# Kernel tuning notes

Measured on AMD Instinct MI355X. Metric: run time of the kernel, lower is better.

The kernel has to match this reference:

```python
import jax, jax.numpy as jnp
import numpy as np

N = 65536      # nodes in batched graph
E = 2097152    # edges (avg degree 32)
V = 1000       # chord vocabulary size
F_IN = 128     # chord feature dim
H = 256        # hidden_dim
OUT = 128      # out_dim
G = 256        # number of graphs in batch


def _gcn_layer(x, W, b, row, col, norm, n):
    # x: [n, f_in] -> [n, f_out]; PyG GCNConv: linear then normalized aggregation + bias
    x = x @ W
    msg = x[row] * norm[:, None]            # gather at source, scale by sym-norm
    return jax.ops.segment_sum(msg, col, num_segments=n) + b


def setup_inputs() -> dict:
    key = jax.random.key(0)
    ks = jax.random.split(key, 9)
    chord_feats = jax.random.normal(ks[0], (V, F_IN), jnp.float32)
    W1 = jax.random.normal(ks[1], (F_IN, H), jnp.float32) * 0.05
    b1 = jnp.zeros((H,), jnp.float32)
    W2 = jax.random.normal(ks[2], (H, OUT), jnp.float32) * 0.05
    b2 = jnp.zeros((OUT,), jnp.float32)
    edge_attr = jax.random.uniform(ks[3], (E,), jnp.float32)          # positive edge weights
    node_indices = jax.random.randint(ks[4], (N,), 0, V, jnp.int64)
    edge_index = jax.random.randint(ks[5], (2, E), 0, N, jnp.int64)
    batch_index = jnp.sort(jax.random.randint(ks[6], (N,), 0, G, jnp.int64))
    return {"chord_feats": chord_feats, "W1": W1, "b1": b1, "W2": W2, "b2": b2,
            "edge_attr": edge_attr, "node_indices": node_indices,
            "edge_index": edge_index, "batch_index": batch_index}


def reference(chord_feats, W1, b1, W2, b2, edge_attr, node_indices, edge_index, batch_index):
    loops = jnp.arange(N, dtype=edge_index.dtype)
    row = jnp.concatenate([edge_index[0], loops])   # source
    col = jnp.concatenate([edge_index[1], loops])   # target
    ew = jnp.concatenate([edge_attr, jnp.ones((N,), edge_attr.dtype)])  # self-loop weight 1
    # symmetric GCN normalization: D^-1/2 A D^-1/2
    deg = jax.ops.segment_sum(ew, col, num_segments=N)
    dis = jnp.where(deg > 0, jax.lax.rsqrt(jnp.maximum(deg, 1e-30)), 0.0)
    norm = dis[row] * ew * dis[col]

    x = chord_feats[node_indices]                   # [N, F_IN]
    x = jax.nn.relu(_gcn_layer(x, W1, b1, row, col, norm, N))
    x = jax.nn.relu(_gcn_layer(x, W2, b2, row, col, norm, N))

    # global_mean_pool over batch_index
    sums = jax.ops.segment_sum(x, batch_index, num_segments=G)
    counts = jax.ops.segment_sum(jnp.ones((N,), x.dtype), batch_index, num_segments=G)
    return sums / jnp.maximum(counts, 1.0)[:, None]
```

## Files before the change

kernel.cpp:

```cpp
#include <hip/hip_runtime.h>
#include <hip/hip_fp16.h>
#include <math.h>

constexpr int N_NODES = 65536;
constexpr int N_EDGES = 2097152;
constexpr int F_IN    = 128;
constexpr int H_DIM   = 256;
constexpr int O_DIM   = 128;
constexpr int N_GRAPH = 256;
constexpr int V_SIZE  = 1000;

constexpr int EPB  = 8192;
constexpr int NBLK = N_EDGES / EPB;
constexpr float FXP = 16777216.0f;

typedef _Float16 half8 __attribute__((ext_vector_type(8)));
typedef float floatx4 __attribute__((ext_vector_type(4)));


__global__ void k_init(float* __restrict__ pool, const int* __restrict__ batch,
                       float* __restrict__ cntf, const float* __restrict__ cf,
                       const float* __restrict__ W1, __half* __restrict__ cfW1,
                       const float* __restrict__ W2, _Float16* __restrict__ W2T) {
    __shared__ float xs[8 * F_IN];
    int i = blockIdx.x * blockDim.x + threadIdx.x;
    if (i < N_GRAPH * O_DIM) pool[i] = 0.0f;
    if (blockIdx.x == 0) {
        int g = threadIdx.x;
        int lo = 0, hi = N_NODES;
        while (lo < hi) { int m = (lo + hi) >> 1; if (batch[m] < g) lo = m + 1; else hi = m; }
        int start = lo;
        lo = 0; hi = N_NODES;
        while (lo < hi) { int m = (lo + hi) >> 1; if (batch[m] <= g) lo = m + 1; else hi = m; }
        cntf[g] = (float)(lo - start);
    }
    if (blockIdx.x < V_SIZE / 8) {
        int rb = blockIdx.x * 8;
        int t  = threadIdx.x;
        #pragma unroll
        for (int p = 0; p < 4; ++p) {
            int idx = p * 256 + t;
            int r = idx >> 7, k = idx & 127;
            xs[idx] = cf[(size_t)(rb + r) * F_IN + k];
        }
        __syncthreads();
        float acc[8] = {};
        for (int k = 0; k < F_IN; ++k) {
            float w = W1[k * H_DIM + t];
            #pragma unroll
            for (int j = 0; j < 8; ++j) acc[j] += xs[j * F_IN + k] * w;
        }
        #pragma unroll
        for (int j = 0; j < 8; ++j)
            cfW1[(size_t)(rb + j) * H_DIM + t] = __float2half(acc[j]);
    }
    if (blockIdx.x >= 128) {
        int idx = (blockIdx.x - 128) * 256 + threadIdx.x;
        int nn = idx >> 8, kk = idx & 255;
        W2T[idx] = (_Float16)W2[kk * O_DIM + nn];
    }
}


__global__ void k_hist(const int* __restrict__ col, int* __restrict__ hist) {
    __shared__ int h[256];
    int t = threadIdx.x;
    if (t < 256) h[t] = 0;
    __syncthreads();
    int base = blockIdx.x * EPB;
    #pragma unroll
    for (int i = 0; i < EPB / 1024; ++i)
        atomicAdd(&h[col[base + i * 1024 + t] >> 8], 1);
    __syncthreads();
    if (t < 256) hist[t * NBLK + blockIdx.x] = h[t];
}


__global__ void k_scan1(const int* __restrict__ in, int* __restrict__ out,
                        int* __restrict__ bsum) {
    __shared__ int s[256];
    int tid = threadIdx.x;
    int i = blockIdx.x * 256 + tid;
    int v = in[i];
    s[tid] = v;
    __syncthreads();
    for (int d = 1; d < 256; d <<= 1) {
        int t = (tid >= d) ? s[tid - d] : 0;
        __syncthreads();
        s[tid] += t;
        __syncthreads();
    }
    out[i] = s[tid] - v;
    if (tid == 255) bsum[blockIdx.x] = s[255];
}

__global__ void k_scan2(int* __restrict__ bsum) {
    __shared__ int s[256];
    int tid = threadIdx.x;
    int v = bsum[tid];
    s[tid] = v;
    __syncthreads();
    for (int d = 1; d < 256; d <<= 1) {
        int t = (tid >= d) ? s[tid - d] : 0;
        __syncthreads();
        s[tid] += t;
        __syncthreads();
    }
    bsum[tid] = s[tid] - v;
}


__global__ void k_part(const int* __restrict__ row, const int* __restrict__ col,
                       const float* __restrict__ ew, const int* __restrict__ nidx,
                       const int* __restrict__ hoffs, const int* __restrict__ bsum,
                       int2* __restrict__ part) {
    __shared__ int cur[256];
    int t = threadIdx.x;
    if (t < 256) cur[t] = hoffs[t * NBLK + blockIdx.x] + bsum[t];
    __syncthreads();
    int base = blockIdx.x * EPB;
    #pragma unroll
    for (int i = 0; i < EPB / 1024; ++i) {
        int e = base + i * 1024 + t;
        int r = row[e], c = col[e];
        unsigned hw = (unsigned)__half_as_ushort(__float2half(ew[e]));
        int vb = nidx[r];
        int slot = atomicAdd(&cur[c >> 8], 1);
        int2 rec;
        rec.x = (r << 16) | ((c & 255) << 8) | (vb >> 2);
        rec.y = (int)(((unsigned)(vb & 3) << 16) | hw);
        part[slot] = rec;
    }
}


__global__ void k_build1(const int* __restrict__ hoffs, const int* __restrict__ bsum,
                         const int2* __restrict__ part, float* __restrict__ dis,
                         int* __restrict__ offs) {
    __shared__ unsigned long long dc[256];
    __shared__ int sc[256];
    int t = threadIdx.x;
    int bucket = blockIdx.x;
    if (t < 256) dc[t] = 0ULL;
    __syncthreads();
    int start = hoffs[bucket * NBLK] + bsum[bucket];
    int end   = (bucket == 255) ? N_EDGES : (hoffs[(bucket + 1) * NBLK] + bsum[bucket + 1]);
    for (int j = start + t; j < end; j += 1024) {
        int2 rec = part[j];
        int dst = (rec.x >> 8) & 255;
        float w = __half2float(__ushort_as_half((unsigned short)(rec.y & 0xFFFF)));
        atomicAdd(&dc[dst], (1ULL << 40) |
                  (unsigned long long)(unsigned)(w * FXP + 0.5f));
    }
    __syncthreads();
    unsigned long long v = (t < 256) ? dc[t] : 0ULL;
    if (t < 256) {
        float deg = 1.0f + (float)(v & 0xFFFFFFFFFFULL) * (1.0f / FXP);
        dis[bucket * 256 + t] = 1.0f / sqrtf(deg);
        sc[t] = (int)(v >> 40);
    }
    __syncthreads();
    for (int d = 1; d < 256; d <<= 1) {
        int x = (t >= d && t < 256) ? sc[t - d] : 0;
        __syncthreads();
        if (t < 256) sc[t] += x;
        __syncthreads();
    }
    if (t < 256) {
        int cnt = (int)(v >> 40);
        offs[bucket * 256 + t] = start + sc[t] - cnt;
    }
    if (bucket == 255 && t == 255) offs[N_NODES] = N_EDGES;
}


__global__ void k_build2(const int* __restrict__ hoffs, const int* __restrict__ bsum,
                         const int2* __restrict__ part, const float* __restrict__ dis,
                         const int* __restrict__ offs, int2* __restrict__ csr) {
    __shared__ int cur[256];
    int t = threadIdx.x;
    int bucket = blockIdx.x;
    if (t < 256) cur[t] = offs[bucket * 256 + t];
    __syncthreads();
    int start = hoffs[bucket * NBLK] + bsum[bucket];
    int end   = (bucket == 255) ? N_EDGES : (hoffs[(bucket + 1) * NBLK] + bsum[bucket + 1]);
    for (int j = start + t; j < end; j += 1024) {
        int2 rec = part[j];
        int dst = (rec.x >> 8) & 255;
        unsigned src = ((unsigned)rec.x) >> 16;
        int vb = ((rec.x & 255) << 2) | ((rec.y >> 16) & 3);
        float w = __half2float(__ushort_as_half((unsigned short)(rec.y & 0xFFFF)));
        float nm = dis[src] * w;
        int slot = atomicAdd(&cur[dst], 1);
        int2 e;
        e.x = (int)((src << 10) | (unsigned)vb);
        e.y = __float_as_int(nm);
        csr[slot] = e;
    }
}

__device__ __forceinline__ void acc8(float* e, int4 v, float n) {
    float2 f0 = __half22float2(*(__half2*)&v.x);
    float2 f1 = __half22float2(*(__half2*)&v.y);
    float2 f2 = __half22float2(*(__half2*)&v.z);
    float2 f3 = __half22float2(*(__half2*)&v.w);
    e[0] += f0.x * n; e[1] += f0.y * n;
    e[2] += f1.x * n; e[3] += f1.y * n;
    e[4] += f2.x * n; e[5] += f2.y * n;
    e[6] += f3.x * n; e[7] += f3.y * n;
}


__global__ void k_agg1(const int4* __restrict__ cfW1, const int* __restrict__ nidx,
                       const float* __restrict__ dis, const int* __restrict__ offs,
                       const int2* __restrict__ csr, const float4* __restrict__ b1f4,
                       int4* __restrict__ h1) {
    int wave = threadIdx.x >> 6;
    int lane = threadIdx.x & 63;
    int g    = lane >> 5;
    int sl   = lane & 31;
    int c = blockIdx.x * 4 + wave;
    float d = dis[c];
    int4 sp = cfW1[(size_t)nidx[c] * 32 + sl];
    float esum[8] = {0.f, 0.f, 0.f, 0.f, 0.f, 0.f, 0.f, 0.f};
    int a0 = offs[c], a1 = offs[c + 1];
    int s = a0;
    if (s < a1 && (s & 1)) {
        int sb = __builtin_amdgcn_readfirstlane(s);
        int2 e0 = csr[sb];
        int4 v0 = cfW1[(size_t)(e0.x & 1023) * 32 + sl];
        float n = (g == 0) ? __int_as_float(e0.y) : 0.0f;
        acc8(esum, v0, n);
        ++s;
    }
    for (; s + 8 <= a1; s += 8) {
        int sb = __builtin_amdgcn_readfirstlane(s);
        int4 ee[4];
        #pragma unroll
        for (int u = 0; u < 4; ++u) ee[u] = *(const int4*)(csr + sb + 2 * u);
        int4 v[4]; float n[4];
        #pragma unroll
        for (int u = 0; u < 4; ++u) {
            int ex = g ? ee[u].z : ee[u].x;
            int ey = g ? ee[u].w : ee[u].y;
            n[u] = __int_as_float(ey);
            v[u] = cfW1[(size_t)(ex & 1023) * 32 + sl];
        }
        #pragma unroll
        for (int u = 0; u < 4; ++u) acc8(esum, v[u], n[u]);
    }
    for (; s + 2 <= a1; s += 2) {
        int sb = __builtin_amdgcn_readfirstlane(s);
        int4 ee = *(const int4*)(csr + sb);
        int ex = g ? ee.z : ee.x;
        int ey = g ? ee.w : ee.y;
        int4 v0 = cfW1[(size_t)(ex & 1023) * 32 + sl];
        acc8(esum, v0, __int_as_float(ey));
    }
    if (s < a1) {
        int sb = __builtin_amdgcn_readfirstlane(s);
        int2 e0 = csr[sb];
        int4 v0 = cfW1[(size_t)(e0.x & 1023) * 32 + sl];
        float n = (g == 0) ? __int_as_float(e0.y) : 0.0f;
        acc8(esum, v0, n);
    }
    #pragma unroll
    for (int k = 0; k < 8; ++k) esum[k] += __shfl_xor(esum[k], 32, 64);

    float dd = d * d;
    float2 s0 = __half22float2(*(__half2*)&sp.x);
    float2 s1 = __half22float2(*(__half2*)&sp.y);
    float2 s2 = __half22float2(*(__half2*)&sp.z);
    float2 s3 = __half22float2(*(__half2*)&sp.w);
    float4 bb0 = b1f4[2 * sl];
    float4 bb1 = b1f4[2 * sl + 1];
    float r[8];
    r[0] = bb0.x + s0.x * dd + d * esum[0];
    r[1] = bb0.y + s0.y * dd + d * esum[1];
    r[2] = bb0.z + s1.x * dd + d * esum[2];
    r[3] = bb0.w + s1.y * dd + d * esum[3];
    r[4] = bb1.x + s2.x * dd + d * esum[4];
    r[5] = bb1.y + s2.y * dd + d * esum[5];
    r[6] = bb1.z + s3.x * dd + d * esum[6];
    r[7] = bb1.w + s3.y * dd + d * esum[7];
    #pragma unroll
    for (int k = 0; k < 8; ++k) r[k] = r[k] > 0.f ? r[k] : 0.f;
    float2 p0 = {r[0], r[1]}, p1 = {r[2], r[3]}, p2 = {r[4], r[5]}, p3 = {r[6], r[7]};
    __half2 h0 = __float22half2_rn(p0);
    __half2 h1v = __float22half2_rn(p1);
    __half2 h2 = __float22half2_rn(p2);
    __half2 h3 = __float22half2_rn(p3);
    int4 outv;
    outv.x = *(int*)&h0;
    outv.y = *(int*)&h1v;
    outv.z = *(int*)&h2;
    outv.w = *(int*)&h3;
    if (lane < 32) h1[(size_t)c * 32 + sl] = outv;
}


__global__ void k_gemm2(const _Float16* __restrict__ h1, const _Float16* __restrict__ W2T,
                        __half* __restrict__ xw2h) {
    int wave = threadIdx.x >> 6;
    int lane = threadIdx.x & 63;
    int quad = lane >> 4;
    int n    = lane & 15;
    int tm   = blockIdx.x * 4 + wave;
    const _Float16* arow = h1 + (size_t)(tm * 16 + n) * H_DIM;
    half8 a[8];
    #pragma unroll
    for (int kt = 0; kt < 8; ++kt)
        a[kt] = *(const half8*)(arow + kt * 32 + quad * 8);
    #pragma unroll
    for (int nt = 0; nt < 8; ++nt) {
        floatx4 acc = {0.f, 0.f, 0.f, 0.f};
        const _Float16* brow = W2T + (size_t)(nt * 16 + n) * H_DIM;
        #pragma unroll
        for (int kt = 0; kt < 8; ++kt) {
            half8 b = *(const half8*)(brow + kt * 32 + quad * 8);
            acc = __builtin_amdgcn_mfma_f32_16x16x32_f16(a[kt], b, acc, 0, 0, 0);
        }
        #pragma unroll
        for (int r = 0; r < 4; ++r) {
            int rowi = tm * 16 + quad * 4 + r;
            xw2h[(size_t)rowi * O_DIM + nt * 16 + n] = __float2half(acc[r]);
        }
    }
}


__global__ void k_agg2_pool(const int4* __restrict__ xw2h, const float* __restrict__ b2,
                            const float* __restrict__ dis, const int* __restrict__ offs,
                            const int2* __restrict__ csr, const int* __restrict__ batch,
                            float* __restrict__ pool) {
    __shared__ float red[4][128];
    __shared__ int bgs[4];
    int wave = threadIdx.x >> 6;
    int lane = threadIdx.x & 63;
    int grp  = lane >> 4;
    int sl   = lane & 15;
    int c = blockIdx.x * 4 + wave;
    float d = dis[c];
    int4 sp = xw2h[(size_t)c * 16 + sl];
    float esum[8] = {0.f, 0.f, 0.f, 0.f, 0.f, 0.f, 0.f, 0.f};
    int s0 = offs[c], s1 = offs[c + 1];
    int s = s0;
    for (; s + 16 <= s1; s += 16) {
        int sb = __builtin_amdgcn_readfirstlane(s);
        int2 e[4];
        #pragma unroll
        for (int u = 0; u < 4; ++u) e[u] = csr[sb + 4 * u + grp];
        int4 v[4];
        #pragma unroll
        for (int u = 0; u < 4; ++u)
            v[u] = xw2h[(size_t)(((unsigned)e[u].x) >> 10) * 16 + sl];
        #pragma unroll
        for (int u = 0; u < 4; ++u) acc8(esum, v[u], __int_as_float(e[u].y));
    }
    for (; s + 4 <= s1; s += 4) {
        int sb = __builtin_amdgcn_readfirstlane(s);
        int2 e0 = csr[sb + grp];
        int4 v0 = xw2h[(size_t)(((unsigned)e0.x) >> 10) * 16 + sl];
        acc8(esum, v0, __int_as_float(e0.y));
    }
    if (s < s1) {
        int sb = __builtin_amdgcn_readfirstlane(s);
        int idx = sb + grp;
        int idc = idx < s1 ? idx : s1 - 1;
        int2 e0 = csr[idc];
        int4 v0 = xw2h[(size_t)(((unsigned)e0.x) >> 10) * 16 + sl];
        float n = (idx < s1) ? __int_as_float(e0.y) : 0.0f;
        acc8(esum, v0, n);
    }
    #pragma unroll
    for (int k = 0; k < 8; ++k) {
        esum[k] += __shfl_xor(esum[k], 16, 64);
        esum[k] += __shfl_xor(esum[k], 32, 64);
    }
    float dd = d * d;
    float2 f0 = __half22float2(*(__half2*)&sp.x);
    float2 f1 = __half22float2(*(__half2*)&sp.y);
    float2 f2 = __half22float2(*(__half2*)&sp.z);
    float2 f3 = __half22float2(*(__half2*)&sp.w);
    float4 bb0 = ((const float4*)b2)[2 * sl];
    float4 bb1 = ((const float4*)b2)[2 * sl + 1];
    float acc[8];
    acc[0] = bb0.x + f0.x * dd + d * esum[0];
    acc[1] = bb0.y + f0.y * dd + d * esum[1];
    acc[2] = bb0.z + f1.x * dd + d * esum[2];
    acc[3] = bb0.w + f1.y * dd + d * esum[3];
    acc[4] = bb1.x + f2.x * dd + d * esum[4];
    acc[5] = bb1.y + f2.y * dd + d * esum[5];
    acc[6] = bb1.z + f3.x * dd + d * esum[6];
    acc[7] = bb1.w + f3.y * dd + d * esum[7];
    #pragma unroll
    for (int k = 0; k < 8; ++k) acc[k] = acc[k] > 0.f ? acc[k] : 0.f;
    if (grp == 0) {
        #pragma unroll
        for (int k = 0; k < 8; ++k) red[wave][8 * sl + k] = acc[k];
    }
    if (lane == 0) bgs[wave] = batch[c];
    __syncthreads();
    if (wave == 0) {
        float2 a;
        a.x = red[0][2 * lane];
        a.y = red[0][2 * lane + 1];
        int cg = bgs[0];
        #pragma unroll
        for (int w = 1; w < 4; ++w) {
            int g = bgs[w];
            float2 r;
            r.x = red[w][2 * lane];
            r.y = red[w][2 * lane + 1];
            if (g == cg) { a.x += r.x; a.y += r.y; }
            else {
                atomicAdd(&pool[cg * O_DIM + 2 * lane], a.x);
                atomicAdd(&pool[cg * O_DIM + 2 * lane + 1], a.y);
                a = r; cg = g;
            }
        }
        atomicAdd(&pool[cg * O_DIM + 2 * lane], a.x);
        atomicAdd(&pool[cg * O_DIM + 2 * lane + 1], a.y);
    }
}

__global__ void k_final(const float* __restrict__ pool, const float* __restrict__ cnt,
                        float* __restrict__ out) {
    int t = blockIdx.x * blockDim.x + threadIdx.x;
    if (t < N_GRAPH * O_DIM) {
        int g = t / O_DIM;
        out[t] = pool[t] / fmaxf(cnt[g], 1.0f);
    }
}


extern "C" void kernel_launch(void* const* d_in, const int* in_sizes, int n_in,
                              void* d_out, int out_size, void* d_ws, size_t ws_size,
                              hipStream_t stream) {
    const float* cf   = (const float*)d_in[0];
    const float* W1   = (const float*)d_in[1];
    const float* b1   = (const float*)d_in[2];
    const float* W2   = (const float*)d_in[3];
    const float* b2   = (const float*)d_in[4];
    const float* ew   = (const float*)d_in[5];
    const int*   nidx = (const int*)d_in[6];
    const int*   eidx = (const int*)d_in[7];
    const int*   bidx = (const int*)d_in[8];
    float* out = (float*)d_out;

    const int* row = eidx;
    const int* col = eidx + N_EDGES;

    char* ws = (char*)d_ws;
    size_t off = 0;
    int*   hist  = (int*)  (ws + off); off += (size_t)N_NODES * 4;
    int*   hoffs = (int*)  (ws + off); off += (size_t)N_NODES * 4;
    int*   bsum  = (int*)  (ws + off); off += 4096;
    float* dis   = (float*)(ws + off); off += (size_t)N_NODES * 4;
    int*   offs  = (int*)  (ws + off); off += (size_t)(N_NODES + 16) * 4;
    int2*  csr   = (int2*) (ws + off); off += (size_t)N_EDGES * 8;
    float* pool  = (float*)(ws + off); off += (size_t)(N_GRAPH * O_DIM + N_GRAPH) * 4;
    __half* cfW1 = (__half*)(ws + off); off += (size_t)V_SIZE * H_DIM * 2;
    _Float16* W2T = (_Float16*)(ws + off); off += (size_t)O_DIM * H_DIM * 2;
    off = (off + 255) & ~(size_t)255;
    int2*  part  = (int2*) (ws + off); off += (size_t)N_EDGES * 8;
    __half* h1   = (__half*)(ws + off);
    __half* xw2h = (__half*)part;
    float* cntf  = pool + N_GRAPH * O_DIM;

    k_init<<<256, 256, 0, stream>>>(pool, bidx, cntf, cf, W1, cfW1, W2, W2T);
    k_hist<<<NBLK, 1024, 0, stream>>>(col, hist);
    k_scan1<<<256, 256, 0, stream>>>(hist, hoffs, bsum);
    k_scan2<<<1, 256, 0, stream>>>(bsum);

    k_part<<<NBLK, 1024, 0, stream>>>(row, col, ew, nidx, hoffs, bsum, part);
    k_build1<<<256, 1024, 0, stream>>>(hoffs, bsum, part, dis, offs);
    k_build2<<<256, 1024, 0, stream>>>(hoffs, bsum, part, dis, offs, csr);

    k_agg1<<<N_NODES / 4, 256, 0, stream>>>((const int4*)cfW1, nidx, dis, offs, csr,
                                            (const float4*)b1, (int4*)h1);

    k_gemm2<<<N_NODES / 64, 256, 0, stream>>>((const _Float16*)h1, W2T, xw2h);
    k_agg2_pool<<<N_NODES / 4, 256, 0, stream>>>((const int4*)xw2h, b2, dis, offs, csr,
                                                 bidx, pool);

    k_final<<<(N_GRAPH * O_DIM + 255) / 256, 256, 0, stream>>>(pool, cntf, out);
}
```

Baseline: 321.3 us.

## Stage partition and CSR scatter through LDS for coalesced writes; fold scan2 into consumers

k_part now builds a block-local histogram and scan, sorts its 8192 records into LDS by bucket, and then writes them to global memory in contiguous bucket runs, replacing random scattered stores. k_build2 also stages each bucket's CSR records in a 10240-entry LDS buffer before a coalesced copy-out, with a fallback to direct scatter for oversized buckets. The separate k_scan2 launch is removed and each consumer block re-scans bsum itself. In exchange, k_part uses a large amount of shared memory and adds extra barriers and scans, which may reduce occupancy.

```diff
diff --git a/kernel.cpp b/kernel.cpp
--- a/kernel.cpp
+++ b/kernel.cpp
@@ -13,6 +13,7 @@
 constexpr int EPB  = 8192;
 constexpr int NBLK = N_EDGES / EPB;
 constexpr float FXP = 16777216.0f;
+constexpr int BUFMAX = 10240;
 
 typedef _Float16 half8 __attribute__((ext_vector_type(8)));
 typedef float floatx4 __attribute__((ext_vector_type(4)));
@@ -94,57 +95,98 @@
     if (tid == 255) bsum[blockIdx.x] = s[255];
 }
 
-__global__ void k_scan2(int* __restrict__ bsum) {
-    __shared__ int s[256];
-    int tid = threadIdx.x;
-    int v = bsum[tid];
-    s[tid] = v;
+__device__ __forceinline__ void scan_bsum(const int* __restrict__ bsum,
+                                          int* __restrict__ sbuf,
+                                          int* __restrict__ exc, int t) {
+    if (t < 256) sbuf[t] = bsum[t];
     __syncthreads();
     for (int d = 1; d < 256; d <<= 1) {
-        int t = (tid >= d) ? s[tid - d] : 0;
-        __syncthreads();
-        s[tid] += t;
-        __syncthreads();
-    }
-    bsum[tid] = s[tid] - v;
-}
-
-
-__global__ void k_part(const int* __restrict__ row, const int* __restrict__ col,
-                       const float* __restrict__ ew, const int* __restrict__ nidx,
-                       const int* __restrict__ hoffs, const int* __restrict__ bsum,
-                       int2* __restrict__ part) {
-    __shared__ int cur[256];
+        int x = (t < 256 && t >= d) ? sbuf[t - d] : 0;
+        __syncthreads();
+        if (t < 256) sbuf[t] += x;
+        __syncthreads();
+    }
+    if (t < 256) exc[t + 1] = sbuf[t];
+    if (t == 0) exc[0] = 0;
+    __syncthreads();
+}
+
+
+__global__ void __launch_bounds__(1024) k_part(
+        const int* __restrict__ row, const int* __restrict__ col,
+        const float* __restrict__ ew, const int* __restrict__ nidx,
+        const int* __restrict__ hoffs, const int* __restrict__ bsum,
+        int2* __restrict__ part) {
+    __shared__ int2 buf[EPB];
+    __shared__ unsigned char sbk[EPB];
+    __shared__ int h[256];
+    __shared__ int lcur[256];
+    __shared__ int wbase[256];
+    __shared__ int sbuf[256];
+    __shared__ int exc[257];
     int t = threadIdx.x;
-    if (t < 256) cur[t] = hoffs[t * NBLK + blockIdx.x] + bsum[t];
-    __syncthreads();
-    int base = blockIdx.x * EPB;
-    #pragma unroll
-    for (int i = 0; i < EPB / 1024; ++i) {
+    int blk = blockIdx.x;
+    scan_bsum(bsum, sbuf, exc, t);
+    if (t < 256) h[t] = 0;
+    __syncthreads();
+    int2 recs[8];
+    int bks[8];
+    int base = blk * EPB;
+    #pragma unroll
+    for (int i = 0; i < 8; ++i) {
         int e = base + i * 1024 + t;
         int r = row[e], c = col[e];
         unsigned hw = (unsigned)__half_as_ushort(__float2half(ew[e]));
         int vb = nidx[r];
-        int slot = atomicAdd(&cur[c >> 8], 1);
-        int2 rec;
-        rec.x = (r << 16) | ((c & 255) << 8) | (vb >> 2);
-        rec.y = (int)(((unsigned)(vb & 3) << 16) | hw);
-        part[slot] = rec;
-    }
-}
-
-
-__global__ void k_build1(const int* __restrict__ hoffs, const int* __restrict__ bsum,
+        recs[i].x = (r << 16) | ((c & 255) << 8) | (vb >> 2);
+        recs[i].y = (int)(((unsigned)(vb & 3) << 16) | hw);
+        bks[i] = c >> 8;
+        atomicAdd(&h[bks[i]], 1);
+    }
+    __syncthreads();
+    if (t < 256) sbuf[t] = h[t];
+    __syncthreads();
+    for (int d = 1; d < 256; d <<= 1) {
+        int x = (t < 256 && t >= d) ? sbuf[t - d] : 0;
+        __syncthreads();
+        if (t < 256) sbuf[t] += x;
+        __syncthreads();
+    }
+    if (t < 256) {
+        int ls = sbuf[t] - h[t];
+        lcur[t] = ls;
+        wbase[t] = hoffs[t * NBLK + blk] + exc[t] - ls;
+    }
+    __syncthreads();
+    #pragma unroll
+    for (int i = 0; i < 8; ++i) {
+        int slot = atomicAdd(&lcur[bks[i]], 1);
+        buf[slot] = recs[i];
+        sbk[slot] = (unsigned char)bks[i];
+    }
+    __syncthreads();
+    #pragma unroll
+    for (int i = 0; i < 8; ++i) {
+        int j = i * 1024 + t;
+        part[wbase[sbk[j]] + j] = buf[j];
+    }
+}
+
+
+__global__ void k_build1(const int* __restrict__ bsum,
                          const int2* __restrict__ part, float* __restrict__ dis,
                          int* __restrict__ offs) {
     __shared__ unsigned long long dc[256];
     __shared__ int sc[256];
+    __shared__ int sbuf[256];
+    __shared__ int exc[257];
     int t = threadIdx.x;
     int bucket = blockIdx.x;
+    scan_bsum(bsum, sbuf, exc, t);
     if (t < 256) dc[t] = 0ULL;
     __syncthreads();
-    int start = hoffs[bucket * NBLK] + bsum[bucket];
-    int end   = (bucket == 255) ? N_EDGES : (hoffs[(bucket + 1) * NBLK] + bsum[bucket + 1]);
+    int start = exc[bucket];
+    int end   = exc[bucket + 1];
     for (int j = start + t; j < end; j += 1024) {
         int2 rec = part[j];
         int dst = (rec.x >> 8) & 255;
@@ -174,28 +216,55 @@
 }
 
 
-__global__ void k_build2(const int* __restrict__ hoffs, const int* __restrict__ bsum,
-                         const int2* __restrict__ part, const float* __restrict__ dis,
-                         const int* __restrict__ offs, int2* __restrict__ csr) {
+__global__ void __launch_bounds__(1024) k_build2(
+        const int* __restrict__ bsum, const int2* __restrict__ part,
+        const float* __restrict__ dis, const int* __restrict__ offs,
+        int2* __restrict__ csr) {
+    __shared__ int2 buf[BUFMAX];
     __shared__ int cur[256];
+    __shared__ int sbuf[256];
+    __shared__ int exc[257];
     int t = threadIdx.x;
     int bucket = blockIdx.x;
-    if (t < 256) cur[t] = offs[bucket * 256 + t];
-    __syncthreads();
-    int start = hoffs[bucket * NBLK] + bsum[bucket];
-    int end   = (bucket == 255) ? N_EDGES : (hoffs[(bucket + 1) * NBLK] + bsum[bucket + 1]);
-    for (int j = start + t; j < end; j += 1024) {
-        int2 rec = part[j];
-        int dst = (rec.x >> 8) & 255;
-        unsigned src = ((unsigned)rec.x) >> 16;
-        int vb = ((rec.x & 255) << 2) | ((rec.y >> 16) & 3);
-        float w = __half2float(__ushort_as_half((unsigned short)(rec.y & 0xFFFF)));
-        float nm = dis[src] * w;
-        int slot = atomicAdd(&cur[dst], 1);
-        int2 e;
-        e.x = (int)((src << 10) | (unsigned)vb);
-        e.y = __float_as_int(nm);
-        csr[slot] = e;
+    scan_bsum(bsum, sbuf, exc, t);
+    int start = exc[bucket];
+    int end   = exc[bucket + 1];
+    int len   = end - start;
+    if (len <= BUFMAX) {
+        if (t < 256) cur[t] = offs[bucket * 256 + t] - start;
+        __syncthreads();
+        for (int j = start + t; j < end; j += 1024) {
+            int2 rec = part[j];
+            int dst = (rec.x >> 8) & 255;
+            unsigned src = ((unsigned)rec.x) >> 16;
+            int vb = ((rec.x & 255) << 2) | ((rec.y >> 16) & 3);
+            float w = __half2float(__ushort_as_half((unsigned short)(rec.y & 0xFFFF)));
+            float nm = dis[src] * w;
+            int slot = atomicAdd(&cur[dst], 1);
+            int2 e;
+            e.x = (int)((src << 10) | (unsigned)vb);
+            e.y = __float_as_int(nm);
+            buf[slot] = e;
+        }
+        __syncthreads();
+        for (int j = t; j < len; j += 1024)
+            csr[start + j] = buf[j];
+    } else {
+        if (t < 256) cur[t] = offs[bucket * 256 + t];
+        __syncthreads();
+        for (int j = start + t; j < end; j += 1024) {
+            int2 rec = part[j];
+            int dst = (rec.x >> 8) & 255;
+            unsigned src = ((unsigned)rec.x) >> 16;
+            int vb = ((rec.x & 255) << 2) | ((rec.y >> 16) & 3);
+            float w = __half2float(__ushort_as_half((unsigned short)(rec.y & 0xFFFF)));
+            float nm = dis[src] * w;
+            int slot = atomicAdd(&cur[dst], 1);
+            int2 e;
+            e.x = (int)((src << 10) | (unsigned)vb);
+            e.y = __float_as_int(nm);
+            csr[slot] = e;
+        }
     }
 }
 
@@ -471,11 +540,10 @@
     k_init<<<256, 256, 0, stream>>>(pool, bidx, cntf, cf, W1, cfW1, W2, W2T);
     k_hist<<<NBLK, 1024, 0, stream>>>(col, hist);
     k_scan1<<<256, 256, 0, stream>>>(hist, hoffs, bsum);
-    k_scan2<<<1, 256, 0, stream>>>(bsum);
 
     k_part<<<NBLK, 1024, 0, stream>>>(row, col, ew, nidx, hoffs, bsum, part);
-    k_build1<<<256, 1024, 0, stream>>>(hoffs, bsum, part, dis, offs);
-    k_build2<<<256, 1024, 0, stream>>>(hoffs, bsum, part, dis, offs, csr);
+    k_build1<<<256, 1024, 0, stream>>>(bsum, part, dis, offs);
+    k_build2<<<256, 1024, 0, stream>>>(bsum, part, dis, offs, csr);
 
     k_agg1<<<N_NODES / 4, 256, 0, stream>>>((const int4*)cfW1, nidx, dis, offs, csr,
                                             (const float4*)b1, (int4*)h1);
```

Result: no change. 315.1 us (-1.9%).
